# Performance work log

Measured on AMD Instinct MI355X. Metric: run time of the kernel, lower is better.

The kernel has to match this reference:

```python
import math
import jax, jax.numpy as jnp
import numpy as np

T_MIN = 0.1
T_MAX = 1.0


def _log_cond_prob(energy, text_mask, mel_mask, direction, neg):
    # energy: (B, I, J); returns (B, I, J, K) with K=J (alpha) or J-1 (beta)
    B, I, J = energy.shape
    if direction == 'alpha':
        K = J
        tri_jk = jnp.arange(J)[:, None] >= jnp.arange(K)[None, :]  # torch triu: valid if j >= k
    else:
        K = J - 1
        tri_jk = jnp.arange(J)[:, None] <= jnp.arange(K)[None, :]  # torch tril: valid if j <= k
    tm = text_mask[:, :, None, None]           # (B,I,1,1)
    mmj = mel_mask[:, None, :, None]           # (B,1,J,1)
    mmk = mel_mask[:, None, None, :K]          # (B,1,1,K)
    mask = tm & mmj & mmk                      # (B,I,J,K)
    tri = tri_jk[None, None] & mask
    mask_invalid = jnp.broadcast_to(tm & mmk, (B, I, J, K))
    text_invalid = jnp.broadcast_to(tm, (B, I, J, K))
    right_mask = mask | (~mask_invalid)
    e = jnp.broadcast_to(energy[..., None], (B, I, J, K))
    e = jnp.where((~tri) & mask_invalid, neg, e)
    e = jnp.where(~mask_invalid, -10.0, e)
    e = e - jax.nn.logsumexp(e, axis=2, keepdims=True)  # normalize over mel dim j
    e = jnp.where(~mask_invalid, neg, e)
    e = jnp.where(~right_mask, -10.0, e)
    e = jnp.where(~text_invalid, -10.0, e)
    return e


def _roll(x, shifts, axis):
    # per-batch roll of x along `axis` by shifts[b]
    return jax.vmap(lambda xb, s: jnp.roll(xb, s, axis=axis - 1))(x, shifts)


def _right_shift(x, sh_t, sh_m):
    x = _roll(x, sh_t, 1)
    x = _roll(x, sh_m, 2)
    return _roll(x, sh_m.at[1:].add(-1), 3)  # faithful to in-place shifts_mel_dim[1:] -= 1


def _left_shift(x, sh_t, sh_m):
    x = x[..., None]
    x = _roll(x, -sh_t, 1)
    x = _roll(x, -sh_m, 2)
    return x[..., 0]


def _compute_alpha(lcp_a, neg):
    # alpha[:, i, j] = lse_k(alpha[:, i-1, k] + lcp_a[:, i-1, j-1, k]) for j >= i
    B, I, J, _ = lcp_a.shape
    j_idx = jnp.arange(J + 1)
    row0 = jnp.full((B, J + 1), neg, dtype=lcp_a.dtype).at[:, 0].set(0.0)

    def step(prev, xs):  # prev = alpha[:, i-1, :J]
        lcp_i, i = xs
        new = jax.nn.logsumexp(prev[:, None, :] + lcp_i, axis=2)  # (B, J), index j-1
        row = jnp.concatenate([jnp.full((B, 1), neg, dtype=new.dtype), new], axis=1)
        row = jnp.where(j_idx[None, :] >= i, row, neg)
        return row[:, :J], row

    _, rows = jax.lax.scan(step, row0[:, :J], (jnp.swapaxes(lcp_a, 0, 1), jnp.arange(1, I + 1)))
    return jnp.concatenate([row0[:, None, :], jnp.swapaxes(rows, 0, 1)], axis=1)  # (B, I+1, J+1)


def _compute_beta(lcp_b, neg):
    # beta[:, i, j] = lse_k(beta[:, i+1, k+1] + lcp_b[:, i, j, k]) for j < J+i-I+1
    B, I, J, _ = lcp_b.shape
    j_idx = jnp.arange(J)
    last = jnp.full((B, J), neg, dtype=lcp_b.dtype).at[:, J - 1].set(0.0)

    def step(nxt, xs):
        lcp_i, i = xs
        full = jax.nn.logsumexp(nxt[:, 1:][:, None, :] + lcp_i, axis=2)  # (B, J)
        row = jnp.where(j_idx[None, :] < (J + i - I + 1), full, neg)
        return row, row

    _, rows = jax.lax.scan(step, last, (jnp.swapaxes(lcp_b[:, :I - 1], 0, 1), jnp.arange(I - 1)), reverse=True)
    return jnp.concatenate([jnp.swapaxes(rows, 0, 1), last[:, None, :]], axis=1)  # (B, I, J)


def _forward(text_embeddings, mel_embeddings, text_mask, mel_mask, noise, temperature_ratio, neg):
    B, I, Dt = text_embeddings.shape
    _, J, Dm = mel_embeddings.shape
    energy = jnp.einsum('bid,bjd->bij', text_embeddings, mel_embeddings) / math.sqrt(Dt * Dm)
    temp = T_MIN + (T_MAX - T_MIN) * temperature_ratio[0]
    energy = (energy - jnp.log(-jnp.log(noise))) / temp  # Gumbel noise + temperature
    lcp_a = _log_cond_prob(energy, text_mask, mel_mask, 'alpha', neg)
    alpha = _compute_alpha(lcp_a, neg)
    t_len = text_mask.sum(1)
    m_len = mel_mask.sum(1)
    sh_t = t_len.max() - t_len
    sh_m = m_len.max() - m_len
    lcp_b = _log_cond_prob(energy, text_mask, mel_mask, 'beta', neg)
    lcp_b = _right_shift(lcp_b, sh_t, sh_m)
    beta = _compute_beta(lcp_b, neg)
    beta = _left_shift(beta, sh_t, sh_m)
    gamma = alpha[:, 1:, 1:] + beta
    gamma_mask = text_mask[:, :, None] & mel_mask[:, None, :]
    gls_mask = jnp.broadcast_to(text_mask[:, :, None], (B, I, J)) | gamma_mask
    gamma = jnp.where(gls_mask, gamma, neg)
    gamma = gamma - jax.nn.logsumexp(gamma, axis=1, keepdims=True)  # normalize over text dim
    gamma = jnp.where(gamma_mask, gamma, neg)
    expanded = jnp.einsum('bij,bid->bjd', jnp.exp(gamma), text_embeddings)
    expanded = expanded * mel_mask[:, :, None]
    return gamma, expanded


def setup_inputs() -> dict:
    key = jax.random.key(0)
    k1, k2, k3, k4 = jax.random.split(key, 4)
    B, I, J, Dt, Dm = 1, 128, 640, 256, 256
    text_embeddings = jax.random.normal(k1, (B, I, Dt), dtype=jnp.float32)
    mel_embeddings = jax.random.normal(k2, (B, J, Dm), dtype=jnp.float32)
    text_mask = jnp.ones((B, I), dtype=bool)
    mel_mask = jnp.ones((B, J), dtype=bool)
    noise = jnp.clip(jax.random.uniform(k3, (B, I, J), dtype=jnp.float32), 1e-8, 1.0 - 1e-8)
    temperature_ratio = jax.random.uniform(k4, (1,), dtype=jnp.float32)
    return {
        'text_embeddings': text_embeddings,
        'mel_embeddings': mel_embeddings,
        'text_mask': text_mask,
        'mel_mask': mel_mask,
        'noise': noise,
        'temperature_ratio': temperature_ratio,
    }


def reference(text_embeddings, mel_embeddings, text_mask, mel_mask, noise, temperature_ratio):
    return _forward(text_embeddings, mel_embeddings, text_mask, mel_mask, noise, temperature_ratio, -jnp.inf)
```

## Files before the change

kernel.cpp:

```cpp
#include <hip/hip_runtime.h>
#include <math.h>

constexpr int TI = 128;
constexpr int TJ = 640;
constexpr int TD = 256;
constexpr int EPL = 10;

#define NEG (-1e30f)
#define LOG2E 1.44269504088896340736f
#define LN2   0.69314718055994530942f

typedef float f32x2 __attribute__((ext_vector_type(2)));
typedef float f32x4 __attribute__((ext_vector_type(4)));

__device__ __forceinline__ float rexp2(float x) { return __builtin_amdgcn_exp2f(x); }
__device__ __forceinline__ float rlog2(float x) { return __builtin_amdgcn_logf(x); }

struct MS { float m, s; };
__device__ __forceinline__ MS ms_combine(MS a, MS b) {
    float d = b.m - a.m;
    bool al = d <= 0.0f;
    float m = al ? a.m : b.m;
    float t = rexp2(al ? d : -d);
    float s = al ? fmaf(b.s, t, a.s) : fmaf(a.s, t, b.s);
    return {m, s};
}
__device__ __forceinline__ MS ms_push(MS run, float x) { return ms_combine(run, {x, 1.0f}); }
__device__ __forceinline__ float ms_final(MS a) {
    return (a.m < -1e29f) ? NEG : a.m + rlog2(a.s);
}

template<int CTRL, int RMASK>
__device__ __forceinline__ float dpp_f(float src, float oldv) {
    int r = __builtin_amdgcn_update_dpp(
        __float_as_int(oldv), __float_as_int(src), CTRL, RMASK, 0xF, false);
    return __int_as_float(r);
}
template<int CTRL, int RMASK>
__device__ __forceinline__ MS dpp_ms(MS v) {
    MS t;
    t.m = dpp_f<CTRL, RMASK>(v.m, NEG);
    t.s = dpp_f<CTRL, RMASK>(v.s, 0.0f);
    return t;
}
__device__ __forceinline__ MS wave_incl_scan_ms(MS v) {
    v = ms_combine(dpp_ms<0x111, 0xF>(v), v);
    v = ms_combine(dpp_ms<0x112, 0xF>(v), v);
    v = ms_combine(dpp_ms<0x114, 0xF>(v), v);
    v = ms_combine(dpp_ms<0x118, 0xF>(v), v);
    v = ms_combine(dpp_ms<0x142, 0xA>(v), v);
    v = ms_combine(dpp_ms<0x143, 0xC>(v), v);
    return v;
}
__device__ __forceinline__ MS wave_excl_from_incl_ms(MS incl) {
    return dpp_ms<0x138, 0xF>(incl);
}
__device__ __forceinline__ float wave_incl_scan_add(float v) {
    v += dpp_f<0x111, 0xF>(v, 0.0f);
    v += dpp_f<0x112, 0xF>(v, 0.0f);
    v += dpp_f<0x114, 0xF>(v, 0.0f);
    v += dpp_f<0x118, 0xF>(v, 0.0f);
    v += dpp_f<0x142, 0xA>(v, 0.0f);
    v += dpp_f<0x143, 0xC>(v, 0.0f);
    return v;
}
__device__ __forceinline__ float wave_incl_scan_max(float v) {
    v = fmaxf(v, dpp_f<0x111, 0xF>(v, NEG));
    v = fmaxf(v, dpp_f<0x112, 0xF>(v, NEG));
    v = fmaxf(v, dpp_f<0x114, 0xF>(v, NEG));
    v = fmaxf(v, dpp_f<0x118, 0xF>(v, NEG));
    v = fmaxf(v, dpp_f<0x142, 0xA>(v, NEG));
    v = fmaxf(v, dpp_f<0x143, 0xC>(v, NEG));
    return v;
}
__device__ __forceinline__ float readlane63(float v) {
    return __int_as_float(__builtin_amdgcn_readlane(__float_as_int(v), 63));
}
__device__ __forceinline__ float readlaneN(float v, int n) {
    return __int_as_float(__builtin_amdgcn_readlane(__float_as_int(v), n));
}

__global__ __launch_bounds__(256) void k_melT(
        const float* __restrict__ mel, float* __restrict__ melT) {
    __shared__ float ldsT[64][65];
    int j0 = blockIdx.x * 64, c0 = blockIdx.y * 64, tid = threadIdx.x;
    int rr = tid >> 4, c4 = tid & 15;
    #pragma unroll
    for (int p = 0; p < 4; p++) {
        int r = p * 16 + rr;
        float4 v = *(const float4*)(mel + (size_t)(j0 + r) * TD + c0 + c4 * 4);
        ldsT[c4 * 4 + 0][r] = v.x;
        ldsT[c4 * 4 + 1][r] = v.y;
        ldsT[c4 * 4 + 2][r] = v.z;
        ldsT[c4 * 4 + 3][r] = v.w;
    }
    __syncthreads();
    int jj = tid & 63, cw = tid >> 6;
    #pragma unroll
    for (int p = 0; p < 16; p++) {
        int cc = p * 4 + cw;
        melT[(size_t)(c0 + cc) * TJ + j0 + jj] = ldsT[cc][jj];
    }
}

__global__ __launch_bounds__(640) void k_energy(
        const float* __restrict__ text, const float* __restrict__ melT,
        const float* __restrict__ noise, const float* __restrict__ trat,
        float* __restrict__ energy, float* __restrict__ Ga,
        float* __restrict__ Gb, float* __restrict__ Cst) {
    __shared__ float trowm[TD], trowc[TD], trowp[TD];
    __shared__ float erowm[TJ], erowc[TJ], erowp[TJ];
    __shared__ float pcur[TJ], scur[TJ];
    __shared__ float wred[2][EPL];
    int i = blockIdx.x, tid = threadIdx.x;
    if (tid < TD) {
        trowc[tid] = text[i * TD + tid];
        trowm[tid] = (i > 0)      ? text[(i - 1) * TD + tid] : 0.0f;
        trowp[tid] = (i < TI - 1) ? text[(i + 1) * TD + tid] : 0.0f;
    }
    __syncthreads();
    float temp = 0.1f + 0.9f * trat[0];
    float sc = LOG2E / temp;
    int j = tid;
    float am = 0.0f, ac = 0.0f, ap = 0.0f;
    #pragma unroll 8
    for (int c = 0; c < TD; c++) {
        float m = melT[(size_t)c * TJ + j];
        am = fmaf(trowm[c], m, am);
        ac = fmaf(trowc[c], m, ac);
        ap = fmaf(trowp[c], m, ap);
    }
    float gm = (i > 0)      ? logf(-logf(noise[(i - 1) * TJ + j])) : 0.0f;
    float gc =                logf(-logf(noise[i * TJ + j]));
    float gp = (i < TI - 1) ? logf(-logf(noise[(i + 1) * TJ + j])) : 0.0f;
    erowm[j] = (am * (1.0f / 256.0f) - gm) * sc;
    float e2 = (ac * (1.0f / 256.0f) - gc) * sc;
    erowc[j] = e2;
    erowp[j] = (ap * (1.0f / 256.0f) - gp) * sc;
    energy[i * TJ + j] = e2;
    __syncthreads();
    if (tid < 64) {
        int l = tid;
        MS loc = {NEG, 0.0f};
        #pragma unroll
        for (int q = 0; q < EPL; q++) loc = ms_push(loc, erowc[l * EPL + q]);
        MS off = wave_excl_from_incl_ms(wave_incl_scan_ms(loc));
        MS run = off;
        #pragma unroll
        for (int q = 0; q < EPL; q++) {
            run = ms_push(run, erowc[l * EPL + q]);
            pcur[l * EPL + q] = ms_final(run);
        }
        loc = {NEG, 0.0f};
        #pragma unroll
        for (int q = 0; q < EPL; q++) loc = ms_push(loc, erowc[TJ - 1 - (l * EPL + q)]);
        off = wave_excl_from_incl_ms(wave_incl_scan_ms(loc));
        run = off;
        #pragma unroll
        for (int q = 0; q < EPL; q++) {
            int idx = TJ - 1 - (l * EPL + q);
            run = ms_push(run, erowc[idx]);
            scur[idx] = ms_final(run);
        }
    }
    __syncthreads();
    float ga, gb;
    if (i == 0) ga = (j == 0) ? -scur[0] : NEG;
    else        ga = (j == 0) ? NEG : erowm[j - 1] - scur[j];
    bool has_b = (i <= TI - 2);
    if (has_b) {
        if (i == TI - 2) gb = (j == 1) ? -pcur[TJ - 2] : NEG;
        else             gb = (j == 0) ? NEG : erowp[TJ - j] - pcur[TJ - 1 - j];
    } else gb = NEG;
    int wv = tid >> 6, l = tid & 63;
    float ma = readlane63(wave_incl_scan_max(ga));
    float mb = readlane63(wave_incl_scan_max(gb));
    if (l == 0) { wred[0][wv] = ma; wred[1][wv] = mb; }
    __syncthreads();
    float Ca = wred[0][0], Cb = wred[1][0];
    #pragma unroll
    for (int k = 1; k < EPL; k++) {
        Ca = fmaxf(Ca, wred[0][k]);
        Cb = fmaxf(Cb, wred[1][k]);
    }
    Ga[i * TJ + j] = rexp2(ga - Ca);
    if (has_b) Gb[i * TJ + j] = rexp2(gb - Cb);
    if (tid == 0) { Cst[i] = Ca; if (has_b) Cst[TI + i] = Cb; }
}

__global__ __launch_bounds__(64, 1) void k_scan(
        const float* __restrict__ Ga, const float* __restrict__ Gb,
        const float* __restrict__ Cst,
        float* __restrict__ PpA, float* __restrict__ PpB,
        float* __restrict__ baseA, float* __restrict__ baseB) {
    constexpr int PF = 7;
    const int l = threadIdx.x;
    const bool is_alpha = (blockIdx.x == 0);
    const int nrows = is_alpha ? TI : TI - 1;
    const float* Gsrc = is_alpha ? Ga : Gb;
    float* Pdst = is_alpha ? PpA : PpB;
    float* bdst = is_alpha ? baseA : baseB;
    const int goff = l * EPL;

#define LOADROW(S, PTR)                                                        \
    asm volatile("global_load_dwordx2 %0, %5, off\n\t"                         \
                 "global_load_dwordx2 %1, %5, off offset:8\n\t"                \
                 "global_load_dwordx2 %2, %5, off offset:16\n\t"               \
                 "global_load_dwordx2 %3, %5, off offset:24\n\t"               \
                 "global_load_dwordx2 %4, %5, off offset:32"                   \
                 : "=&v"(gr[S][0]), "=&v"(gr[S][1]), "=&v"(gr[S][2]),          \
                   "=&v"(gr[S][3]), "=&v"(gr[S][4])                            \
                 : "v"(PTR))

    float C0, C1;
    {
        const float* c0p = Cst + (is_alpha ? 0 : 128) + l;
        const float* c1p = c0p + 64;
        asm volatile("global_load_dword %0, %2, off\n\t"
                     "global_load_dword %1, %3, off"
                     : "=&v"(C0), "=&v"(C1) : "v"(c0p), "v"(c1p));
        asm volatile("s_waitcnt vmcnt(0)" ::: "memory");
        __builtin_amdgcn_sched_barrier(0);
    }

    f32x2 gr[PF][5];
    {
        const float* gp0 = Gsrc + (size_t)(is_alpha ? 0 : TI - 2) * TJ + goff;
        const float* gp1 = Gsrc + (size_t)(is_alpha ? 1 : TI - 3) * TJ + goff;
        const float* gp2 = Gsrc + (size_t)(is_alpha ? 2 : TI - 4) * TJ + goff;
        const float* gp3 = Gsrc + (size_t)(is_alpha ? 3 : TI - 5) * TJ + goff;
        const float* gp4 = Gsrc + (size_t)(is_alpha ? 4 : TI - 6) * TJ + goff;
        const float* gp5 = Gsrc + (size_t)(is_alpha ? 5 : TI - 7) * TJ + goff;
        const float* gp6 = Gsrc + (size_t)(is_alpha ? 6 : TI - 8) * TJ + goff;
        LOADROW(0, gp0); LOADROW(1, gp1); LOADROW(2, gp2); LOADROW(3, gp3);
        LOADROW(4, gp4); LOADROW(5, gp5); LOADROW(6, gp6);
    }

    float Pp[EPL];
    #pragma unroll
    for (int q = 0; q < EPL; q++) Pp[q] = 0.0f;
    float rprev = 0.0f, Lam = 0.0f;
    float bacc0 = 0.0f, bacc1 = 0.0f;

#define ROWBODY(S, T, KLIT, IS_FIRST)                                          \
    {                                                                          \
        asm volatile("s_waitcnt vmcnt(" KLIT ")" ::: "memory");                \
        __builtin_amdgcn_sched_barrier(0);                                     \
        float gv[EPL];                                                         \
        _Pragma("unroll")                                                      \
        for (int k = 0; k < 5; k++) {                                          \
            gv[2 * k] = gr[S][k][0]; gv[2 * k + 1] = gr[S][k][1];              \
        }                                                                      \
        {   \
            int tp = (T) + PF;                                                 \
            int rpi = (tp < nrows) ? tp : (nrows - 1);                         \
            int rowp = is_alpha ? rpi : (TI - 2 - rpi);                        \
            const float* gpn = Gsrc + (size_t)rowp * TJ + goff;                \
            LOADROW(S, gpn);                                                   \
        }                                                                      \
        float lp[EPL];                                                         \
        if (IS_FIRST) {                                                        \
            _Pragma("unroll")                                                  \
            for (int q = 0; q < EPL; q++) lp[q] = gv[q];                       \
        } else {                                                               \
            float carry = dpp_f<0x138, 0xF>(Pp[EPL - 1], 0.0f);                \
            float rp = rprev;                                                  \
            lp[0] = carry * rp * gv[0];                                        \
            _Pragma("unroll")                                                  \
            for (int q = 1; q < EPL; q++) lp[q] = Pp[q - 1] * rp * gv[q];      \
        }                                                                      \
        _Pragma("unroll")                                                      \
        for (int q = 9; q >= 1; q--) lp[q] += lp[q - 1];                       \
        _Pragma("unroll")                                                      \
        for (int q = 9; q >= 2; q--) lp[q] += lp[q - 2];                       \
        _Pragma("unroll")                                                      \
        for (int q = 9; q >= 4; q--) lp[q] += lp[q - 4];                       \
        _Pragma("unroll")                                                      \
        for (int q = 9; q >= 8; q--) lp[q] += lp[q - 8];                       \
        float incl = wave_incl_scan_add(lp[EPL - 1]);                          \
        float excl = dpp_f<0x138, 0xF>(incl, 0.0f);                            \
        _Pragma("unroll")                                                      \
        for (int q = 0; q < EPL; q++) Pp[q] = excl + lp[q];                    \
        float T_ = readlane63(incl);                                           \
        int idx2 = is_alpha ? (T) : (126 - (T));                               \
        float Cc = (idx2 < 64) ? readlaneN(C0, idx2)                           \
                               : readlaneN(C1, idx2 - 64);                     \
        float basev = Lam + Cc;                                                \
        {            \
            f32x4 p03, p47; f32x2 p89;                                         \
            p03[0] = Pp[0]; p03[1] = Pp[1]; p03[2] = Pp[2]; p03[3] = Pp[3];    \
            p47[0] = Pp[4]; p47[1] = Pp[5]; p47[2] = Pp[6]; p47[3] = Pp[7];    \
            p89[0] = Pp[8]; p89[1] = Pp[9];                                    \
            float* pp = Pdst + (size_t)(T) * TJ + goff;                        \
            asm volatile("global_store_dwordx4 %0, %1, off\n\t"                \
                         "global_store_dwordx4 %0, %2, off offset:16\n\t"      \
                         "global_store_dwordx2 %0, %3, off offset:32"          \
                         :: "v"(pp), "v"(p03), "v"(p47), "v"(p89) : "memory"); \
        }                                                                      \
        bacc0 = ((T) == l)      ? basev : bacc0;                               \
        bacc1 = ((T) == 64 + l) ? basev : bacc1;                               \
        Lam = basev + rlog2(T_);                                               \
        rprev = (T_ > 0.0f) ? __builtin_amdgcn_rcpf(T_) : 0.0f;                \
    }

    ROWBODY(0, 0, "30", true);
    ROWBODY(1, 1, "33", false);
    ROWBODY(2, 2, "36", false);
    ROWBODY(3, 3, "39", false);
    ROWBODY(4, 4, "42", false);
    ROWBODY(5, 5, "45", false);
    ROWBODY(6, 6, "48", false);

    for (int tb = PF; tb < nrows; tb += PF) {
        { int t = tb + 0; if (t < nrows) ROWBODY(0, t, "51", false); }
        { int t = tb + 1; if (t < nrows) ROWBODY(1, t, "51", false); }
        { int t = tb + 2; if (t < nrows) ROWBODY(2, t, "51", false); }
        { int t = tb + 3; if (t < nrows) ROWBODY(3, t, "51", false); }
        { int t = tb + 4; if (t < nrows) ROWBODY(4, t, "51", false); }
        { int t = tb + 5; if (t < nrows) ROWBODY(5, t, "51", false); }
        { int t = tb + 6; if (t < nrows) ROWBODY(6, t, "51", false); }
    }

    asm volatile("s_waitcnt vmcnt(0)" ::: "memory");
    __builtin_amdgcn_sched_barrier(0);
    bdst[l] = bacc0;
    bdst[64 + l] = bacc1;
#undef ROWBODY
#undef LOADROW
}

__global__ __launch_bounds__(256) void k_gamma(
        const float* __restrict__ PpA, const float* __restrict__ PpB,
        const float* __restrict__ baseA, const float* __restrict__ baseB,
        const float* __restrict__ energy, const float* __restrict__ text,
        float* __restrict__ outg, float* __restrict__ oute) {
    __shared__ float w128[TI];
    __shared__ float redm[2], reds[2];
    int j = blockIdx.x, tid = threadIdx.x;
    float gg = NEG;
    if (tid < TI) {
        float ev = energy[tid * TJ + j];
        float av = ev + rlog2(PpA[tid * TJ + j]) + baseA[tid];
        float bv;
        if (tid == TI - 1) {
            bv = (j == TJ - 1) ? 0.0f : NEG;
        } else {
            int t = TI - 2 - tid;
            bv = ev + rlog2(PpB[(size_t)t * TJ + (TJ - 1 - j)]) + baseB[t];
        }
        gg = (av < -1e29f || bv < -1e29f) ? NEG : av + bv;
        MS v = {gg, 1.0f};
        #pragma unroll
        for (int off = 32; off > 0; off >>= 1) {
            float om = __shfl_xor(v.m, off, 64);
            float os = __shfl_xor(v.s, off, 64);
            v = ms_combine(v, {om, os});
        }
        if ((tid & 63) == 0) { redm[tid >> 6] = v.m; reds[tid >> 6] = v.s; }
    }
    __syncthreads();
    float lse = ms_final(ms_combine({redm[0], reds[0]}, {redm[1], reds[1]}));
    if (tid < TI) {
        bool fin = gg > -1e29f;
        outg[tid * TJ + j] = fin ? (gg - lse) * LN2 : NEG;
        w128[tid] = fin ? rexp2(gg - lse) : 0.0f;
    }
    __syncthreads();
    float acc = 0.0f;
    #pragma unroll 8
    for (int ii = 0; ii < TI; ii++) acc += w128[ii] * text[ii * TD + tid];
    oute[(size_t)j * TD + tid] = acc;
}

extern "C" void kernel_launch(void* const* d_in, const int* in_sizes, int n_in,
                              void* d_out, int out_size, void* d_ws, size_t ws_size,
                              hipStream_t stream) {
    const float* text  = (const float*)d_in[0];
    const float* mel   = (const float*)d_in[1];
    const float* noise = (const float*)d_in[4];
    const float* trat  = (const float*)d_in[5];

    float* outg = (float*)d_out;
    float* oute = outg + TI * TJ;

    float* w      = (float*)d_ws;
    float* energy = w;
    float* Ga     = w + 1 * TI * TJ;
    float* Gb     = w + 2 * TI * TJ;
    float* Cst    = Gb + (size_t)(TI - 1) * TJ;
    float* baseA  = Cst + 320;
    float* baseB  = Cst + 448;
    float* melT   = w + 3 * TI * TJ;
    float* PpA    = w + 3 * TI * TJ;
    float* PpB    = w + 4 * TI * TJ;

    k_melT  <<<dim3(TJ / 64, TD / 64), 256, 0, stream>>>(mel, melT);
    k_energy<<<TI, TJ, 0, stream>>>(text, melT, noise, trat, energy, Ga, Gb, Cst);
    k_scan  <<<2, 64, 0, stream>>>(Ga, Gb, Cst, PpA, PpB, baseA, baseB);
    k_gamma <<<TJ, 256, 0, stream>>>(PpA, PpB, baseA, baseB, energy, text, outg, oute);
}
```

Measured before the change: 124.9 us.

## Permute G/P row layout for coalesced dwordx4 loads and deepen scan prefetch

```diff
diff --git a/kernel.cpp b/kernel.cpp
--- a/kernel.cpp
+++ b/kernel.cpp
@@ -15,6 +15,12 @@
 
 __device__ __forceinline__ float rexp2(float x) { return __builtin_amdgcn_exp2f(x); }
 __device__ __forceinline__ float rlog2(float x) { return __builtin_amdgcn_logf(x); }
+
+__device__ __forceinline__ int permP(int j) {
+    int l = j / 10, qq = j - l * 10;
+    return (qq < 8) ? ((qq >> 2) * 256 + l * 4 + (qq & 3))
+                    : (512 + l * 2 + (qq - 8));
+}
 
 struct MS { float m, s; };
 __device__ __forceinline__ MS ms_combine(MS a, MS b) {
@@ -183,8 +189,9 @@
         Ca = fmaxf(Ca, wred[0][k]);
         Cb = fmaxf(Cb, wred[1][k]);
     }
-    Ga[i * TJ + j] = rexp2(ga - Ca);
-    if (has_b) Gb[i * TJ + j] = rexp2(gb - Cb);
+    int pj = permP(j);
+    Ga[i * TJ + pj] = rexp2(ga - Ca);
+    if (has_b) Gb[i * TJ + pj] = rexp2(gb - Cb);
     if (tid == 0) { Cst[i] = Ca; if (has_b) Cst[TI + i] = Cb; }
 }
 
@@ -193,24 +200,22 @@
         const float* __restrict__ Cst,
         float* __restrict__ PpA, float* __restrict__ PpB,
         float* __restrict__ baseA, float* __restrict__ baseB) {
-    constexpr int PF = 7;
+    constexpr int PF = 8;
     const int l = threadIdx.x;
     const bool is_alpha = (blockIdx.x == 0);
     const int nrows = is_alpha ? TI : TI - 1;
     const float* Gsrc = is_alpha ? Ga : Gb;
     float* Pdst = is_alpha ? PpA : PpB;
     float* bdst = is_alpha ? baseA : baseB;
-    const int goff = l * EPL;
-
-#define LOADROW(S, PTR)                                                        \
-    asm volatile("global_load_dwordx2 %0, %5, off\n\t"                         \
-                 "global_load_dwordx2 %1, %5, off offset:8\n\t"                \
-                 "global_load_dwordx2 %2, %5, off offset:16\n\t"               \
-                 "global_load_dwordx2 %3, %5, off offset:24\n\t"               \
-                 "global_load_dwordx2 %4, %5, off offset:32"                   \
-                 : "=&v"(gr[S][0]), "=&v"(gr[S][1]), "=&v"(gr[S][2]),          \
-                   "=&v"(gr[S][3]), "=&v"(gr[S][4])                            \
-                 : "v"(PTR))
+    const int o16 = l * 16;
+    const int o8  = l * 8;
+
+#define LOADROW(S, RPTR)                                                       \
+    asm volatile("global_load_dwordx4 %0, %3, %5\n\t"                          \
+                 "global_load_dwordx4 %1, %3, %5 offset:1024\n\t"              \
+                 "global_load_dwordx2 %2, %4, %5 offset:2048"                  \
+                 : "=&v"(g4a[S]), "=&v"(g4b[S]), "=&v"(g2[S])                  \
+                 : "v"(o16), "v"(o8), "s"(RPTR))
 
     float C0, C1;
     {
@@ -223,17 +228,19 @@
         __builtin_amdgcn_sched_barrier(0);
     }
 
-    f32x2 gr[PF][5];
+    f32x4 g4a[PF], g4b[PF];
+    f32x2 g2[PF];
     {
-        const float* gp0 = Gsrc + (size_t)(is_alpha ? 0 : TI - 2) * TJ + goff;
-        const float* gp1 = Gsrc + (size_t)(is_alpha ? 1 : TI - 3) * TJ + goff;
-        const float* gp2 = Gsrc + (size_t)(is_alpha ? 2 : TI - 4) * TJ + goff;
-        const float* gp3 = Gsrc + (size_t)(is_alpha ? 3 : TI - 5) * TJ + goff;
-        const float* gp4 = Gsrc + (size_t)(is_alpha ? 4 : TI - 6) * TJ + goff;
-        const float* gp5 = Gsrc + (size_t)(is_alpha ? 5 : TI - 7) * TJ + goff;
-        const float* gp6 = Gsrc + (size_t)(is_alpha ? 6 : TI - 8) * TJ + goff;
-        LOADROW(0, gp0); LOADROW(1, gp1); LOADROW(2, gp2); LOADROW(3, gp3);
-        LOADROW(4, gp4); LOADROW(5, gp5); LOADROW(6, gp6);
+        const float* r0 = Gsrc + (size_t)(is_alpha ? 0 : TI - 2) * TJ;
+        const float* r1 = Gsrc + (size_t)(is_alpha ? 1 : TI - 3) * TJ;
+        const float* r2 = Gsrc + (size_t)(is_alpha ? 2 : TI - 4) * TJ;
+        const float* r3 = Gsrc + (size_t)(is_alpha ? 3 : TI - 5) * TJ;
+        const float* r4 = Gsrc + (size_t)(is_alpha ? 4 : TI - 6) * TJ;
+        const float* r5 = Gsrc + (size_t)(is_alpha ? 5 : TI - 7) * TJ;
+        const float* r6 = Gsrc + (size_t)(is_alpha ? 6 : TI - 8) * TJ;
+        const float* r7 = Gsrc + (size_t)(is_alpha ? 7 : TI - 9) * TJ;
+        LOADROW(0, r0); LOADROW(1, r1); LOADROW(2, r2); LOADROW(3, r3);
+        LOADROW(4, r4); LOADROW(5, r5); LOADROW(6, r6); LOADROW(7, r7);
     }
 
     float Pp[EPL];
@@ -247,15 +254,16 @@
         asm volatile("s_waitcnt vmcnt(" KLIT ")" ::: "memory");                \
         __builtin_amdgcn_sched_barrier(0);                                     \
         float gv[EPL];                                                         \
-        _Pragma("unroll")                                                      \
-        for (int k = 0; k < 5; k++) {                                          \
-            gv[2 * k] = gr[S][k][0]; gv[2 * k + 1] = gr[S][k][1];              \
-        }                                                                      \
+        gv[0] = g4a[S][0]; gv[1] = g4a[S][1];                                  \
+        gv[2] = g4a[S][2]; gv[3] = g4a[S][3];                                  \
+        gv[4] = g4b[S][0]; gv[5] = g4b[S][1];                                  \
+        gv[6] = g4b[S][2]; gv[7] = g4b[S][3];                                  \
+        gv[8] = g2[S][0];  gv[9] = g2[S][1];                                   \
         {   \
             int tp = (T) + PF;                                                 \
             int rpi = (tp < nrows) ? tp : (nrows - 1);                         \
             int rowp = is_alpha ? rpi : (TI - 2 - rpi);                        \
-            const float* gpn = Gsrc + (size_t)rowp * TJ + goff;                \
+            const float* gpn = Gsrc + (size_t)rowp * TJ;                       \
             LOADROW(S, gpn);                                                   \
         }                                                                      \
         float lp[EPL];                                                         \
@@ -286,16 +294,17 @@
         float Cc = (idx2 < 64) ? readlaneN(C0, idx2)                           \
                                : readlaneN(C1, idx2 - 64);                     \
         float basev = Lam + Cc;                                                \
-        {            \
+        {                \
             f32x4 p03, p47; f32x2 p89;                                         \
             p03[0] = Pp[0]; p03[1] = Pp[1]; p03[2] = Pp[2]; p03[3] = Pp[3];    \
             p47[0] = Pp[4]; p47[1] = Pp[5]; p47[2] = Pp[6]; p47[3] = Pp[7];    \
             p89[0] = Pp[8]; p89[1] = Pp[9];                                    \
-            float* pp = Pdst + (size_t)(T) * TJ + goff;                        \
-            asm volatile("global_store_dwordx4 %0, %1, off\n\t"                \
-                         "global_store_dwordx4 %0, %2, off offset:16\n\t"      \
-                         "global_store_dwordx2 %0, %3, off offset:32"          \
-                         :: "v"(pp), "v"(p03), "v"(p47), "v"(p89) : "memory"); \
+            float* pp = Pdst + (size_t)(T) * TJ;                               \
+            asm volatile("global_store_dwordx4 %0, %2, %5\n\t"                 \
+                         "global_store_dwordx4 %0, %3, %5 offset:1024\n\t"     \
+                         "global_store_dwordx2 %1, %4, %5 offset:2048"         \
+                         :: "v"(o16), "v"(o8), "v"(p03), "v"(p47), "v"(p89),   \
+                            "s"(pp) : "memory");                               \
         }                                                                      \
         bacc0 = ((T) == l)      ? basev : bacc0;                               \
         bacc1 = ((T) == 64 + l) ? basev : bacc1;                               \
@@ -303,22 +312,24 @@
         rprev = (T_ > 0.0f) ? __builtin_amdgcn_rcpf(T_) : 0.0f;                \
     }
 
-    ROWBODY(0, 0, "30", true);
-    ROWBODY(1, 1, "33", false);
-    ROWBODY(2, 2, "36", false);
-    ROWBODY(3, 3, "39", false);
-    ROWBODY(4, 4, "42", false);
-    ROWBODY(5, 5, "45", false);
-    ROWBODY(6, 6, "48", false);
+    ROWBODY(0, 0, "21", true);
+    ROWBODY(1, 1, "24", false);
+    ROWBODY(2, 2, "27", false);
+    ROWBODY(3, 3, "30", false);
+    ROWBODY(4, 4, "33", false);
+    ROWBODY(5, 5, "36", false);
+    ROWBODY(6, 6, "39", false);
+    ROWBODY(7, 7, "42", false);
 
     for (int tb = PF; tb < nrows; tb += PF) {
-        { int t = tb + 0; if (t < nrows) ROWBODY(0, t, "51", false); }
-        { int t = tb + 1; if (t < nrows) ROWBODY(1, t, "51", false); }
-        { int t = tb + 2; if (t < nrows) ROWBODY(2, t, "51", false); }
-        { int t = tb + 3; if (t < nrows) ROWBODY(3, t, "51", false); }
-        { int t = tb + 4; if (t < nrows) ROWBODY(4, t, "51", false); }
-        { int t = tb + 5; if (t < nrows) ROWBODY(5, t, "51", false); }
-        { int t = tb + 6; if (t < nrows) ROWBODY(6, t, "51", false); }
+        { int t = tb + 0; if (t < nrows) ROWBODY(0, t, "45", false); }
+        { int t = tb + 1; if (t < nrows) ROWBODY(1, t, "45", false); }
+        { int t = tb + 2; if (t < nrows) ROWBODY(2, t, "45", false); }
+        { int t = tb + 3; if (t < nrows) ROWBODY(3, t, "45", false); }
+        { int t = tb + 4; if (t < nrows) ROWBODY(4, t, "45", false); }
+        { int t = tb + 5; if (t < nrows) ROWBODY(5, t, "45", false); }
+        { int t = tb + 6; if (t < nrows) ROWBODY(6, t, "45", false); }
+        { int t = tb + 7; if (t < nrows) ROWBODY(7, t, "45", false); }
     }
 
     asm volatile("s_waitcnt vmcnt(0)" ::: "memory");
@@ -337,16 +348,18 @@
     __shared__ float w128[TI];
     __shared__ float redm[2], reds[2];
     int j = blockIdx.x, tid = threadIdx.x;
+    int offA = permP(j);
+    int offB = permP(TJ - 1 - j);
     float gg = NEG;
     if (tid < TI) {
         float ev = energy[tid * TJ + j];
-        float av = ev + rlog2(PpA[tid * TJ + j]) + baseA[tid];
+        float av = ev + rlog2(PpA[tid * TJ + offA]) + baseA[tid];
         float bv;
         if (tid == TI - 1) {
             bv = (j == TJ - 1) ? 0.0f : NEG;
         } else {
             int t = TI - 2 - tid;
-            bv = ev + rlog2(PpB[(size_t)t * TJ + (TJ - 1 - j)]) + baseB[t];
+            bv = ev + rlog2(PpB[(size_t)t * TJ + offB]) + baseB[t];
         }
         gg = (av < -1e29f || bv < -1e29f) ? NEG : av + bv;
         MS v = {gg, 1.0f};
```

Measured after the change: 123.9 us. About the same (-0.8%).
